# Kernel optimization log

Measured on AMD Instinct MI355X. Metric: run time of the kernel, lower is better.

## Reference

```python
import jax, jax.numpy as jnp
import numpy as np

B, S, H = 4, 2048, 1024
HEADS = 16
DFF = 4 * H
EPS = 1e-12


def _layer_norm(x, w, b):
    mu = jnp.mean(x, axis=-1, keepdims=True)
    var = jnp.mean(jnp.square(x - mu), axis=-1, keepdims=True)
    return (x - mu) * jax.lax.rsqrt(var + EPS) * w + b


def setup_inputs() -> dict:
    key = jax.random.key(0)
    ks = jax.random.split(key, 12)
    sc = 0.02
    return {
        "input": jax.random.normal(ks[0], (B, S, H), dtype=jnp.float32),
        "input_mask": jnp.zeros((B, 1, 1, S), dtype=jnp.float32),
        "norm_w": jnp.ones((H,), jnp.float32),
        "norm_b": jnp.zeros((H,), jnp.float32),
        "qkv_w": sc * jax.random.normal(ks[1], (H, 3 * H), jnp.float32),
        "qkv_b": jnp.zeros((3 * H,), jnp.float32),
        "attn_ow": sc * jax.random.normal(ks[2], (H, H), jnp.float32),
        "attn_ob": jnp.zeros((H,), jnp.float32),
        "attn_nw": jnp.ones((H,), jnp.float32),
        "attn_nb": jnp.zeros((H,), jnp.float32),
        "inter_w": sc * jax.random.normal(ks[3], (H, DFF), jnp.float32),
        "inter_b": jnp.zeros((DFF,), jnp.float32),
        "output_w": sc * jax.random.normal(ks[4], (DFF, H), jnp.float32),
        "output_b": jnp.zeros((H,), jnp.float32),
    }


def reference(input, input_mask, norm_w, norm_b, qkv_w, qkv_b, attn_ow, attn_ob,
              attn_nw, attn_nb, inter_w, inter_b, output_w, output_b):
    b, s, h = input.shape
    hd = h // HEADS
    # pre-LN + fused QKV projection (qkv_func)
    x_ln = _layer_norm(input, norm_w, norm_b)
    qkv = x_ln @ qkv_w + qkv_b                      # [b, s, 3h]
    qkv = qkv.reshape(b, s, 3, HEADS, hd)
    q, k, v = qkv[:, :, 0], qkv[:, :, 1], qkv[:, :, 2]   # [b, s, heads, hd]
    # scaled dot-product attention (flash_attn equivalent, non-causal)
    scale = 1.0 / jnp.sqrt(jnp.float32(hd))
    scores = jnp.einsum('bqnd,bknd->bnqk', q, k) * scale  # [b, heads, s, s]
    scores = scores + input_mask                           # additive mask
    probs = jax.nn.softmax(scores, axis=-1)
    ctx = jnp.einsum('bnqk,bknd->bqnd', probs, v).reshape(b, s, h)
    # attention output projection + residual (mlp_func first half)
    attn_out = ctx @ attn_ow + attn_ob + input
    # post-attention LN + FFN (GELU) + residual
    y = _layer_norm(attn_out, attn_nw, attn_nb)
    y = jax.nn.gelu(y @ inter_w + inter_b, approximate=False)
    return y @ output_w + output_b + attn_out
```

## Files before the change

### kernel.cpp

```cpp
#include <hip/hip_runtime.h>
#include <math.h>

typedef __bf16 bf16_t;
typedef bf16_t bf16x8 __attribute__((ext_vector_type(8)));
typedef bf16_t bf16x4 __attribute__((ext_vector_type(4)));
typedef float f32x4 __attribute__((ext_vector_type(4)));
typedef float f32x16 __attribute__((ext_vector_type(16)));

#define BB 4
#define SS 2048
#define HD1 1024
#define NH 16
#define DFF_ 4096

__device__ __forceinline__ void gload_lds16(const bf16_t* g, bf16_t* l) {
  __builtin_amdgcn_global_load_lds(
      (const __attribute__((address_space(1))) void*)g,
      (__attribute__((address_space(3))) void*)l, 16, 0, 0);
}

__device__ __forceinline__ unsigned pack2_bf16(float a, float b) {
  union { bf16_t h[2]; unsigned u; } cv;
  cv.h[0] = (bf16_t)a;
  cv.h[1] = (bf16_t)b;
  return cv.u;
}

__device__ __forceinline__ float block_reduce_sum(float v, float* red) {
  const int lane = threadIdx.x & 63;
  const int wid = threadIdx.x >> 6;
#pragma unroll
  for (int off = 32; off > 0; off >>= 1) v += __shfl_down(v, off, 64);
  if (lane == 0) red[wid] = v;
  __syncthreads();
  float s = red[0] + red[1] + red[2] + red[3];
  __syncthreads();
  return s;
}

__global__ __launch_bounds__(256) void ln_kernel(const float* __restrict__ x,
                                                 const float* __restrict__ w,
                                                 const float* __restrict__ bv,
                                                 bf16_t* __restrict__ out) {
  __shared__ float red[4];
  const size_t row = blockIdx.x;
  const float4 xv = *(const float4*)(x + row * HD1 + threadIdx.x * 4);
  float s = xv.x + xv.y + xv.z + xv.w;
  s = block_reduce_sum(s, red);
  const float mu = s * (1.0f / HD1);
  float4 d;
  d.x = xv.x - mu; d.y = xv.y - mu; d.z = xv.z - mu; d.w = xv.w - mu;
  float sq = d.x * d.x + d.y * d.y + d.z * d.z + d.w * d.w;
  sq = block_reduce_sum(sq, red);
  const float rs = rsqrtf(sq * (1.0f / HD1) + 1e-12f);
  const float4 wv = *(const float4*)(w + threadIdx.x * 4);
  const float4 bb = *(const float4*)(bv + threadIdx.x * 4);
  bf16x4 o;
  o[0] = (bf16_t)(d.x * rs * wv.x + bb.x);
  o[1] = (bf16_t)(d.y * rs * wv.y + bb.y);
  o[2] = (bf16_t)(d.z * rs * wv.z + bb.z);
  o[3] = (bf16_t)(d.w * rs * wv.w + bb.w);
  *(bf16x4*)(out + row * HD1 + threadIdx.x * 4) = o;
}

__global__ __launch_bounds__(256) void wt_kernel(const float* __restrict__ W,
                                                 bf16_t* __restrict__ Wt,
                                                 int K, int N) {
  __shared__ bf16_t T[32][33];
  const int t = threadIdx.x;
  const int n0 = blockIdx.x * 32, k0 = blockIdx.y * 32;
  const int a = t >> 5, c = t & 31;
#pragma unroll
  for (int i = 0; i < 4; ++i) {
    const int kl = a + i * 8;
    T[kl][c] = (bf16_t)W[(size_t)(k0 + kl) * N + n0 + c];
  }
  __syncthreads();
#pragma unroll
  for (int i = 0; i < 4; ++i) {
    const int nl = a + i * 8;
    Wt[(size_t)(n0 + nl) * K + k0 + c] = T[c][nl];
  }
}

__global__ __launch_bounds__(256) void vtrans_kernel(const bf16_t* __restrict__ qkv,
                                                     bf16_t* __restrict__ Vt) {
  const int t = threadIdx.x;
  const int s = blockIdx.x * 256 + t;
  const int head = blockIdx.y, b = blockIdx.z;
  const bf16_t* src = qkv + (size_t)(b * SS + s) * 3072 + 2048 + head * 64;
  bf16_t* dst = Vt + ((size_t)(b * NH + head) * 64) * SS + s;
#pragma unroll
  for (int j = 0; j < 8; ++j) {
    bf16x8 v = *(const bf16x8*)(src + j * 8);
#pragma unroll
    for (int e = 0; e < 8; ++e) dst[(size_t)(j * 8 + e) * SS] = v[e];
  }
}

#define BAR() __builtin_amdgcn_s_barrier()
#define LGKM0()                                         \
  do {                                                  \
    asm volatile("s_waitcnt lgkmcnt(0)" ::: "memory");  \
    __builtin_amdgcn_sched_barrier(0);                  \
  } while (0)
#define VM4 asm volatile("s_waitcnt vmcnt(4)" ::: "memory")
#define VM0 asm volatile("s_waitcnt vmcnt(0)" ::: "memory")
#define PRIO1 __builtin_amdgcn_s_setprio(1)
#define PRIO0 __builtin_amdgcn_s_setprio(0)

template <int EPI, bool OBF>
__global__ __launch_bounds__(512) void gemm8p(
    const bf16_t* __restrict__ A, const bf16_t* __restrict__ Wt,
    const float* __restrict__ bias, const float* __restrict__ R,
    void* __restrict__ Cout, int M, int N, int K) {
  __shared__ __align__(16) char smem[98304];
  bf16_t* As = (bf16_t*)smem;
  bf16_t* Bs = (bf16_t*)(smem + 32768);

  const int tid = threadIdx.x;
  const int lane = tid & 63;
  const int w = tid >> 6;
  const int l15 = lane & 15, l4 = lane >> 4;
  const int wr = w >> 2;
  const int wc = w & 3;
  const int bh = wc >> 1;
  const int bro = (wc & 1) * 64;

  const int gx = gridDim.x;
  int id = blockIdx.x + gx * blockIdx.y;
  const int cpx = (gx * gridDim.y) >> 3;
  id = (id & 7) * cpx + (id >> 3);
  const int m0 = (id / gx) * 128;
  const int n0 = (id % gx) * 256;

  const int srow = tid >> 3;
  const int scol = (((tid & 7) ^ ((tid >> 3) & 7)) * 8);
  const bf16_t* Ag = A + (size_t)(m0 + srow) * K + scol;
  const bf16_t* Bg = Wt + (size_t)(n0 + srow) * K + scol;
  const size_t K64 = (size_t)64 * K;

  const int chA0 = ((l4) ^ (l15 & 7)) * 8;
  const int chA1 = ((4 + l4) ^ (l15 & 7)) * 8;

#define STA(d, h, t)                                                       \
  gload_lds16(Ag + (size_t)(h)*64 * K + (size_t)(t)*64,                    \
              As + (d)*8192 + (h)*4096 + w * 512)
#define STB(d, h, t)                                                       \
  do {                                                                     \
    gload_lds16(Bg + (size_t)(h)*128 * K + (size_t)(t)*64,                 \
                Bs + (d)*16384 + (h)*8192 + w * 512);                      \
    gload_lds16(Bg + (size_t)(h)*128 * K + K64 + (size_t)(t)*64,           \
                Bs + (d)*16384 + (h)*8192 + 4096 + w * 512);               \
  } while (0)

  bf16x8 af[4][2], bfr[4][2];
  f32x4 acc[4][4] = {};

#define LDA(cur)                                                           \
  do {                                                                     \
    const bf16_t* Ah_ = As + (cur)*8192 + wr * 4096;                       \
    _Pragma("unroll") for (int i_ = 0; i_ < 4; ++i_) {                     \
      af[i_][0] = *(const bf16x8*)(Ah_ + (i_ * 16 + l15) * 64 + chA0);     \
      af[i_][1] = *(const bf16x8*)(Ah_ + (i_ * 16 + l15) * 64 + chA1);     \
    }                                                                      \
  } while (0)
#define LDB(cur, j0)                                                       \
  do {                                                                     \
    const bf16_t* Bh_ = Bs + (cur)*16384 + bh * 8192;                      \
    _Pragma("unroll") for (int j_ = (j0); j_ < (j0) + 2; ++j_) {           \
      bfr[j_][0] = *(const bf16x8*)(Bh_ + (bro + j_ * 16 + l15) * 64 + chA0); \
      bfr[j_][1] = *(const bf16x8*)(Bh_ + (bro + j_ * 16 + l15) * 64 + chA1); \
    }                                                                      \
  } while (0)
#define MM(i0, j0)                                                         \
  do {                                                                     \
    _Pragma("unroll") for (int ks_ = 0; ks_ < 2; ++ks_)                    \
    _Pragma("unroll") for (int i_ = 0; i_ < 2; ++i_)                       \
    _Pragma("unroll") for (int j_ = 0; j_ < 2; ++j_)                       \
        acc[(i0) + i_][(j0) + j_] = __builtin_amdgcn_mfma_f32_16x16x32_bf16( \
            af[(i0) + i_][ks_], bfr[(j0) + j_][ks_],                       \
            acc[(i0) + i_][(j0) + j_], 0, 0, 0);                           \
  } while (0)

  STA(0, 0, 0); STA(0, 1, 0); STB(0, 0, 0); STB(0, 1, 0);
  STA(1, 0, 1); STA(1, 1, 1); STB(1, 0, 1);
  VM4;
  BAR();

  const int NT = K >> 6;
  const int nIter = NT >> 1;
  for (int it = 0; it < nIter; ++it) {
    const int u = 2 * it;
    const bool lastI = (it == nIter - 1);
    LDA(0);
    LDB(0, 0);
    STB(1, 1, u + 1);
    BAR(); LGKM0(); PRIO1; MM(0, 0); PRIO0; BAR();
    LDB(0, 2);
    if (!lastI) STA(0, 0, u + 2);
    BAR(); LGKM0(); PRIO1; MM(2, 0); PRIO0; BAR();
    if (!lastI) STA(0, 1, u + 2);
    BAR(); PRIO1; MM(0, 2); PRIO0; BAR();
    if (!lastI) { STB(0, 0, u + 2); VM4; } else { VM0; }
    BAR(); PRIO1; MM(2, 2); PRIO0; BAR();
    LDA(1);
    LDB(1, 0);
    if (!lastI) STB(0, 1, u + 2);
    BAR(); LGKM0(); PRIO1; MM(0, 0); PRIO0; BAR();
    LDB(1, 2);
    if (!lastI) STA(1, 0, u + 3);
    BAR(); LGKM0(); PRIO1; MM(2, 0); PRIO0; BAR();
    if (!lastI) STA(1, 1, u + 3);
    BAR(); PRIO1; MM(0, 2); PRIO0; BAR();
    if (!lastI) { STB(1, 0, u + 3); VM4; }
    BAR(); PRIO1; MM(2, 2); PRIO0; BAR();
  }
#undef STA
#undef STB
#undef LDA
#undef LDB
#undef MM

  if (OBF) {
    float* Cs = (float*)smem;
    bf16_t* Cb = (bf16_t*)Cout;
    __syncthreads();
#pragma unroll
    for (int p = 0; p < 2; ++p) {
      if (p) __syncthreads();
      if (wr == p) {
#pragma unroll
        for (int i = 0; i < 4; ++i) {
#pragma unroll
          for (int j = 0; j < 4; ++j) {
            const int col = wc * 64 + j * 16 + l15;
            const float bj = bias[n0 + col];
#pragma unroll
            for (int r = 0; r < 4; ++r) {
              float v = acc[i][j][r] + bj;
              if (EPI == 1)
                v = 0.5f * v * (1.0f + erff(v * 0.70710678118654752440f));
              const int lr = i * 16 + l4 * 4 + r;
              const int q = (((col >> 2) ^ (lr & 7)) << 2);
              Cs[lr * 256 + q + (col & 3)] = v;
            }
          }
        }
      }
      __syncthreads();
      const int orow = tid >> 3;
      const int oc = tid & 7;
#pragma unroll
      for (int k = 0; k < 4; ++k) {
        const int col = k * 64 + oc * 8;
        const int q0 = ((((col >> 2) + 0) ^ (orow & 7)) << 2);
        const int q1 = ((((col >> 2) + 1) ^ (orow & 7)) << 2);
        const f32x4 v0 = *(const f32x4*)(Cs + orow * 256 + q0);
        const f32x4 v1 = *(const f32x4*)(Cs + orow * 256 + q1);
        bf16x8 o;
        o[0] = (bf16_t)v0[0]; o[1] = (bf16_t)v0[1];
        o[2] = (bf16_t)v0[2]; o[3] = (bf16_t)v0[3];
        o[4] = (bf16_t)v1[0]; o[5] = (bf16_t)v1[1];
        o[6] = (bf16_t)v1[2]; o[7] = (bf16_t)v1[3];
        *(bf16x8*)(Cb + (size_t)(m0 + p * 64 + orow) * N + n0 + col) = o;
      }
    }
  } else {
    float* Cf = (float*)Cout;
#pragma unroll
    for (int j = 0; j < 4; ++j) {
      const int gn = n0 + wc * 64 + j * 16 + l15;
      const float bj = bias[gn];
#pragma unroll
      for (int i = 0; i < 4; ++i) {
        const int gm = m0 + wr * 64 + i * 16 + l4 * 4;
#pragma unroll
        for (int r = 0; r < 4; ++r) {
          float v = acc[i][j][r] + bj;
          if (EPI == 2) v += R[(size_t)(gm + r) * N + gn];
          Cf[(size_t)(gm + r) * N + gn] = v;
        }
      }
    }
  }
}

__global__ __launch_bounds__(256, 2) void attn_kernel(
    const bf16_t* __restrict__ qkv, const bf16_t* __restrict__ Vt,
    const float* __restrict__ mask, bf16_t* __restrict__ ctx) {
  __shared__ __align__(16) bf16_t K_lds[64 * 72];
  __shared__ __align__(16) bf16_t Vt_lds[64 * 72];
  const int tid = threadIdx.x;
  const int lane = tid & 63;
  const int w = tid >> 6;
  const int l31 = lane & 31;
  const int h = lane >> 5;
  const int q0 = blockIdx.x * 128;
  const int head = blockIdx.y;
  const int b = blockIdx.z;
  const int qrow = q0 + w * 32 + l31;

  bf16x8 qf[4];
  {
    const bf16_t* qp = qkv + (size_t)(b * SS + qrow) * 3072 + head * 64 + 8 * h;
#pragma unroll
    for (int ks = 0; ks < 4; ++ks) qf[ks] = *(const bf16x8*)(qp + 16 * ks);
  }

  const int srow = tid >> 2;
  const int scol = (tid & 3) * 16;

  float m = -3.0e38f, l = 0.0f;
  f32x16 cacc0 = {};
  f32x16 cacc1 = {};

  for (int kv0 = 0; kv0 < SS; kv0 += 64) {
    const bf16_t* kp =
        qkv + (size_t)(b * SS + kv0 + srow) * 3072 + 1024 + head * 64 + scol;
    const bf16_t* vp =
        Vt + ((size_t)(b * NH + head) * 64 + srow) * SS + kv0 + scol;
    const bf16x8 k0 = *(const bf16x8*)kp;
    const bf16x8 k1 = *(const bf16x8*)(kp + 8);
    const bf16x8 v0 = *(const bf16x8*)vp;
    const bf16x8 v1 = *(const bf16x8*)(vp + 8);
    float4 mv[8];
#pragma unroll
    for (int k2 = 0; k2 < 8; ++k2)
      mv[k2] = *(const float4*)(mask + (size_t)b * SS + kv0 + 8 * k2 + 4 * h);
    __syncthreads();
    *(bf16x8*)(K_lds + srow * 72 + scol) = k0;
    *(bf16x8*)(K_lds + srow * 72 + scol + 8) = k1;
    *(bf16x8*)(Vt_lds + srow * 72 + scol) = v0;
    *(bf16x8*)(Vt_lds + srow * 72 + scol + 8) = v1;
    __syncthreads();

    f32x16 sacc0 = {};
    f32x16 sacc1 = {};
#pragma unroll
    for (int ks = 0; ks < 4; ++ks) {
      const bf16x8 kf0 = *(const bf16x8*)(K_lds + l31 * 72 + 16 * ks + 8 * h);
      const bf16x8 kf1 =
          *(const bf16x8*)(K_lds + (l31 + 32) * 72 + 16 * ks + 8 * h);
      sacc0 = __builtin_amdgcn_mfma_f32_32x32x16_bf16(kf0, qf[ks], sacc0, 0, 0, 0);
      sacc1 = __builtin_amdgcn_mfma_f32_32x32x16_bf16(kf1, qf[ks], sacc1, 0, 0, 0);
    }

    float ps[32];
    float tmax = -3.0e38f;
#pragma unroll
    for (int r = 0; r < 16; ++r) {
      const float s0 = sacc0[r] * 0.125f + mv[(r >> 2)][r & 3];
      const float s1 = sacc1[r] * 0.125f + mv[(r >> 2) + 4][r & 3];
      ps[r] = s0;
      ps[16 + r] = s1;
      tmax = fmaxf(tmax, fmaxf(s0, s1));
    }
    tmax = fmaxf(tmax, __shfl_xor(tmax, 32, 64));
    if (__any(tmax > m + 8.0f)) {
      const float mnew = fmaxf(m, tmax);
      const float sc = __expf(m - mnew);
      m = mnew;
      l *= sc;
#pragma unroll
      for (int r = 0; r < 16; ++r) {
        const float scr = __shfl(sc, (r & 3) + 8 * (r >> 2) + 4 * h, 64);
        cacc0[r] *= scr;
        cacc1[r] *= scr;
      }
    }
    float ls = 0.0f;
#pragma unroll
    for (int i = 0; i < 32; ++i) {
      ps[i] = __expf(ps[i] - m);
      ls += ps[i];
    }
    l += ls + __shfl_xor(ls, 32, 64);

    unsigned pw0[8], pw1[8];
#pragma unroll
    for (int k = 0; k < 8; ++k) {
      const int base = (k >> 2) * 16 + (k & 3) * 4;
      pw0[k] = pack2_bf16(ps[base + 0], ps[base + 1]);
      pw1[k] = pack2_bf16(ps[base + 2], ps[base + 3]);
    }
#pragma unroll
    for (int t = 0; t < 4; ++t) {
      const unsigned e0 = h ? pw0[2 * t] : pw0[2 * t + 1];
      const unsigned e1 = h ? pw1[2 * t] : pw1[2 * t + 1];
      const unsigned o0 = (unsigned)__shfl_xor((int)e0, 32, 64);
      const unsigned o1 = (unsigned)__shfl_xor((int)e1, 32, 64);
      const unsigned a0 = h ? pw0[2 * t + 1] : pw0[2 * t];
      const unsigned a1 = h ? pw1[2 * t + 1] : pw1[2 * t];
      union { unsigned u[4]; bf16x8 v; } pu;
      pu.u[0] = h ? o0 : a0;
      pu.u[1] = h ? o1 : a1;
      pu.u[2] = h ? a0 : o0;
      pu.u[3] = h ? a1 : o1;
      const bf16x8 vf0 = *(const bf16x8*)(Vt_lds + l31 * 72 + 16 * t + 8 * h);
      const bf16x8 vf1 =
          *(const bf16x8*)(Vt_lds + (l31 + 32) * 72 + 16 * t + 8 * h);
      cacc0 = __builtin_amdgcn_mfma_f32_32x32x16_bf16(pu.v, vf0, cacc0, 0, 0, 0);
      cacc1 = __builtin_amdgcn_mfma_f32_32x32x16_bf16(pu.v, vf1, cacc1, 0, 0, 0);
    }
  }

  const float linv = 1.0f / l;
#pragma unroll
  for (int r = 0; r < 16; ++r) {
    const int rq = (r & 3) + 8 * (r >> 2) + 4 * h;
    const float li = __shfl(linv, rq, 64);
    const int grow = q0 + w * 32 + rq;
    bf16_t* op = ctx + (size_t)(b * SS + grow) * 1024 + head * 64 + l31;
    op[0] = (bf16_t)(cacc0[r] * li);
    op[32] = (bf16_t)(cacc1[r] * li);
  }
}

extern "C" void kernel_launch(void* const* d_in, const int* in_sizes, int n_in,
                              void* d_out, int out_size, void* d_ws, size_t ws_size,
                              hipStream_t stream) {
  const float* input    = (const float*)d_in[0];
  const float* mask     = (const float*)d_in[1];
  const float* norm_w   = (const float*)d_in[2];
  const float* norm_b   = (const float*)d_in[3];
  const float* qkv_w    = (const float*)d_in[4];
  const float* qkv_b    = (const float*)d_in[5];
  const float* attn_ow  = (const float*)d_in[6];
  const float* attn_ob  = (const float*)d_in[7];
  const float* attn_nw  = (const float*)d_in[8];
  const float* attn_nb  = (const float*)d_in[9];
  const float* inter_w  = (const float*)d_in[10];
  const float* inter_b  = (const float*)d_in[11];
  const float* output_w = (const float*)d_in[12];
  const float* output_b = (const float*)d_in[13];

  char* ws = (char*)d_ws;
  const size_t off_xln = 0;
  const size_t off_qkv = 16777216;
  const size_t off_vt  = 67108864;
  const size_t off_ctx = 83886080;
  const size_t off_ao  = 100663296;
  const size_t off_wq  = 134217728;
  const size_t off_wo  = 140509184;
  const size_t off_wi  = 142606336;
  const size_t off_w2  = 150994944;
  const size_t NEED    = 159383552;
  if (ws_size < NEED) return;

  bf16_t* x_ln  = (bf16_t*)(ws + off_xln);
  bf16_t* qkvb  = (bf16_t*)(ws + off_qkv);
  bf16_t* VtB   = (bf16_t*)(ws + off_vt);
  bf16_t* ctxb  = (bf16_t*)(ws + off_ctx);
  bf16_t* y_ln  = (bf16_t*)(ws + off_ctx);
  float*  a_out = (float*)(ws + off_ao);
  bf16_t* wq_t  = (bf16_t*)(ws + off_wq);
  bf16_t* wo_t  = (bf16_t*)(ws + off_wo);
  bf16_t* wi_t  = (bf16_t*)(ws + off_wi);
  bf16_t* w2_t  = (bf16_t*)(ws + off_w2);
  bf16_t* act   = (bf16_t*)(ws + off_xln);

  const int M = BB * SS;

  wt_kernel<<<dim3(3072 / 32, 1024 / 32), 256, 0, stream>>>(qkv_w, wq_t, 1024, 3072);
  wt_kernel<<<dim3(1024 / 32, 1024 / 32), 256, 0, stream>>>(attn_ow, wo_t, 1024, 1024);
  wt_kernel<<<dim3(4096 / 32, 1024 / 32), 256, 0, stream>>>(inter_w, wi_t, 1024, 4096);
  wt_kernel<<<dim3(1024 / 32, 4096 / 32), 256, 0, stream>>>(output_w, w2_t, 4096, 1024);

  ln_kernel<<<M, 256, 0, stream>>>(input, norm_w, norm_b, x_ln);
  gemm8p<0, true><<<dim3(3072 / 256, M / 128), 512, 0, stream>>>(
      x_ln, wq_t, qkv_b, nullptr, qkvb, M, 3072, 1024);
  vtrans_kernel<<<dim3(SS / 256, NH, BB), 256, 0, stream>>>(qkvb, VtB);
  attn_kernel<<<dim3(SS / 128, NH, BB), 256, 0, stream>>>(qkvb, VtB, mask, ctxb);
  gemm8p<2, false><<<dim3(1024 / 256, M / 128), 512, 0, stream>>>(
      ctxb, wo_t, attn_ob, input, a_out, M, 1024, 1024);
  ln_kernel<<<M, 256, 0, stream>>>(a_out, attn_nw, attn_nb, y_ln);
  gemm8p<1, true><<<dim3(4096 / 256, M / 128), 512, 0, stream>>>(
      y_ln, wi_t, inter_b, nullptr, act, M, 4096, 1024);
  gemm8p<2, false><<<dim3(1024 / 256, M / 128), 512, 0, stream>>>(
      act, w2_t, output_b, a_out, (float*)d_out, M, 1024, 4096);
}
```

Measured before the change: 547.4 us.

## Enlarge GEMM block tile to 256x256 with 8x4 per-warp accumulators

The bf16 GEMM block tile grows from 128x256 to 256x256. Each warp now computes a 128x64 sub-tile with 32 accumulators, and LDS double-buffering is reorganised (128KB shared memory) with a new fragment load and MFMA interleave and adjusted vmcnt waits. The aim is higher arithmetic intensity per LDS and global load and half as many blocks. In exchange register pressure and LDS use rise, which lowers occupancy, and the M=1024 GEMMs get fewer blocks (128), which may underfill the 256 CUs.

```diff
diff --git a/kernel.cpp b/kernel.cpp
--- a/kernel.cpp
+++ b/kernel.cpp
@@ -104,7 +104,8 @@
     asm volatile("s_waitcnt lgkmcnt(0)" ::: "memory");  \
     __builtin_amdgcn_sched_barrier(0);                  \
   } while (0)
-#define VM4 asm volatile("s_waitcnt vmcnt(4)" ::: "memory")
+#define VM8 asm volatile("s_waitcnt vmcnt(8)" ::: "memory")
+#define VM6 asm volatile("s_waitcnt vmcnt(6)" ::: "memory")
 #define VM0 asm volatile("s_waitcnt vmcnt(0)" ::: "memory")
 #define PRIO1 __builtin_amdgcn_s_setprio(1)
 #define PRIO0 __builtin_amdgcn_s_setprio(0)
@@ -114,9 +115,9 @@
     const bf16_t* __restrict__ A, const bf16_t* __restrict__ Wt,
     const float* __restrict__ bias, const float* __restrict__ R,
     void* __restrict__ Cout, int M, int N, int K) {
-  __shared__ __align__(16) char smem[98304];
-  bf16_t* As = (bf16_t*)smem;
-  bf16_t* Bs = (bf16_t*)(smem + 32768);
+  __shared__ __align__(16) char smem[131072];
+  bf16_t* As0 = (bf16_t*)smem;
+  bf16_t* Bs0 = (bf16_t*)(smem + 65536);
 
   const int tid = threadIdx.x;
   const int lane = tid & 63;
@@ -124,68 +125,88 @@
   const int l15 = lane & 15, l4 = lane >> 4;
   const int wr = w >> 2;
   const int wc = w & 3;
-  const int bh = wc >> 1;
-  const int bro = (wc & 1) * 64;
 
   const int gx = gridDim.x;
   int id = blockIdx.x + gx * blockIdx.y;
   const int cpx = (gx * gridDim.y) >> 3;
   id = (id & 7) * cpx + (id >> 3);
-  const int m0 = (id / gx) * 128;
+  const int m0 = (id / gx) * 256;
   const int n0 = (id % gx) * 256;
 
   const int srow = tid >> 3;
   const int scol = (((tid & 7) ^ ((tid >> 3) & 7)) * 8);
   const bf16_t* Ag = A + (size_t)(m0 + srow) * K + scol;
   const bf16_t* Bg = Wt + (size_t)(n0 + srow) * K + scol;
-  const size_t K64 = (size_t)64 * K;
-
-  const int chA0 = ((l4) ^ (l15 & 7)) * 8;
-  const int chA1 = ((4 + l4) ^ (l15 & 7)) * 8;
-
-#define STA(d, h, t)                                                       \
-  gload_lds16(Ag + (size_t)(h)*64 * K + (size_t)(t)*64,                    \
-              As + (d)*8192 + (h)*4096 + w * 512)
-#define STB(d, h, t)                                                       \
-  do {                                                                     \
-    gload_lds16(Bg + (size_t)(h)*128 * K + (size_t)(t)*64,                 \
-                Bs + (d)*16384 + (h)*8192 + w * 512);                      \
-    gload_lds16(Bg + (size_t)(h)*128 * K + K64 + (size_t)(t)*64,           \
-                Bs + (d)*16384 + (h)*8192 + 4096 + w * 512);               \
-  } while (0)
-
-  bf16x8 af[4][2], bfr[4][2];
-  f32x4 acc[4][4] = {};
-
-#define LDA(cur)                                                           \
-  do {                                                                     \
-    const bf16_t* Ah_ = As + (cur)*8192 + wr * 4096;                       \
-    _Pragma("unroll") for (int i_ = 0; i_ < 4; ++i_) {                     \
-      af[i_][0] = *(const bf16x8*)(Ah_ + (i_ * 16 + l15) * 64 + chA0);     \
-      af[i_][1] = *(const bf16x8*)(Ah_ + (i_ * 16 + l15) * 64 + chA1);     \
-    }                                                                      \
-  } while (0)
-#define LDB(cur, j0)                                                       \
-  do {                                                                     \
-    const bf16_t* Bh_ = Bs + (cur)*16384 + bh * 8192;                      \
-    _Pragma("unroll") for (int j_ = (j0); j_ < (j0) + 2; ++j_) {           \
-      bfr[j_][0] = *(const bf16x8*)(Bh_ + (bro + j_ * 16 + l15) * 64 + chA0); \
-      bfr[j_][1] = *(const bf16x8*)(Bh_ + (bro + j_ * 16 + l15) * 64 + chA1); \
-    }                                                                      \
-  } while (0)
-#define MM(i0, j0)                                                         \
-  do {                                                                     \
-    _Pragma("unroll") for (int ks_ = 0; ks_ < 2; ++ks_)                    \
-    _Pragma("unroll") for (int i_ = 0; i_ < 2; ++i_)                       \
-    _Pragma("unroll") for (int j_ = 0; j_ < 2; ++j_)                       \
-        acc[(i0) + i_][(j0) + j_] = __builtin_amdgcn_mfma_f32_16x16x32_bf16( \
-            af[(i0) + i_][ks_], bfr[(j0) + j_][ks_],                       \
-            acc[(i0) + i_][(j0) + j_], 0, 0, 0);                           \
-  } while (0)
-
-  STA(0, 0, 0); STA(0, 1, 0); STB(0, 0, 0); STB(0, 1, 0);
-  STA(1, 0, 1); STA(1, 1, 1); STB(1, 0, 1);
-  VM4;
+
+#define STGA(d, h, t)                                                     \
+  do {                                                                    \
+    gload_lds16(Ag + (size_t)((h)*128) * K + (size_t)(t)*64,              \
+                As0 + (d)*16384 + (h)*8192 + w * 512);                    \
+    gload_lds16(Ag + (size_t)((h)*128 + 64) * K + (size_t)(t)*64,         \
+                As0 + (d)*16384 + (h)*8192 + 4096 + w * 512);             \
+  } while (0)
+#define STGB(d, h, t)                                                     \
+  do {                                                                    \
+    gload_lds16(Bg + (size_t)((h)*128) * K + (size_t)(t)*64,              \
+                Bs0 + (d)*16384 + (h)*8192 + w * 512);                    \
+    gload_lds16(Bg + (size_t)((h)*128 + 64) * K + (size_t)(t)*64,         \
+                Bs0 + (d)*16384 + (h)*8192 + 4096 + w * 512);             \
+  } while (0)
+
+  const int rdA = (wr * 128 + l15) * 64;
+  const int rdB = (wc * 64 + l15) * 64;
+  const int ch0 = ((l4) ^ (l15 & 7)) * 8;
+  const int ch1 = ((4 + l4) ^ (l15 & 7)) * 8;
+
+  bf16x8 afA[4][2], afB[4][2], bfA[2][2], bfB[2][2];
+  f32x4 acc[8][4] = {};
+
+#define LDA03(d)                                                          \
+  do {                                                                    \
+    const bf16_t* p_ = As0 + (d)*16384 + rdA;                             \
+    _Pragma("unroll") for (int i_ = 0; i_ < 4; ++i_) {                    \
+      afA[i_][0] = *(const bf16x8*)(p_ + i_ * 1024 + ch0);                \
+      afA[i_][1] = *(const bf16x8*)(p_ + i_ * 1024 + ch1);                \
+    }                                                                     \
+  } while (0)
+#define LDA47(d)                                                          \
+  do {                                                                    \
+    const bf16_t* p_ = As0 + (d)*16384 + rdA + 4096;                      \
+    _Pragma("unroll") for (int i_ = 0; i_ < 4; ++i_) {                    \
+      afB[i_][0] = *(const bf16x8*)(p_ + i_ * 1024 + ch0);                \
+      afB[i_][1] = *(const bf16x8*)(p_ + i_ * 1024 + ch1);                \
+    }                                                                     \
+  } while (0)
+#define LDB01(d)                                                          \
+  do {                                                                    \
+    const bf16_t* p_ = Bs0 + (d)*16384 + rdB;                             \
+    _Pragma("unroll") for (int j_ = 0; j_ < 2; ++j_) {                    \
+      bfA[j_][0] = *(const bf16x8*)(p_ + j_ * 1024 + ch0);                \
+      bfA[j_][1] = *(const bf16x8*)(p_ + j_ * 1024 + ch1);                \
+    }                                                                     \
+  } while (0)
+#define LDB23(d)                                                          \
+  do {                                                                    \
+    const bf16_t* p_ = Bs0 + (d)*16384 + rdB + 2048;                      \
+    _Pragma("unroll") for (int j_ = 0; j_ < 2; ++j_) {                    \
+      bfB[j_][0] = *(const bf16x8*)(p_ + j_ * 1024 + ch0);                \
+      bfB[j_][1] = *(const bf16x8*)(p_ + j_ * 1024 + ch1);                \
+    }                                                                     \
+  } while (0)
+#define MMQ(AF, BF, IO, JO)                                               \
+  do {                                                                    \
+    _Pragma("unroll") for (int ks_ = 0; ks_ < 2; ++ks_)                   \
+    _Pragma("unroll") for (int i_ = 0; i_ < 4; ++i_)                      \
+    _Pragma("unroll") for (int j_ = 0; j_ < 2; ++j_)                      \
+        acc[(IO) + i_][(JO) + j_] =                                       \
+            __builtin_amdgcn_mfma_f32_16x16x32_bf16(                      \
+                AF[i_][ks_], BF[j_][ks_], acc[(IO) + i_][(JO) + j_],      \
+                0, 0, 0);                                                 \
+  } while (0)
+
+  STGA(0, 0, 0); STGA(0, 1, 0); STGB(0, 0, 0); STGB(0, 1, 0);
+  STGA(1, 0, 1); STGA(1, 1, 1); STGB(1, 0, 1); STGB(1, 1, 1);
+  VM8;
   BAR();
 
   const int NT = K >> 6;
@@ -193,34 +214,34 @@
   for (int it = 0; it < nIter; ++it) {
     const int u = 2 * it;
     const bool lastI = (it == nIter - 1);
-    LDA(0);
-    LDB(0, 0);
-    STB(1, 1, u + 1);
-    BAR(); LGKM0(); PRIO1; MM(0, 0); PRIO0; BAR();
-    LDB(0, 2);
-    if (!lastI) STA(0, 0, u + 2);
-    BAR(); LGKM0(); PRIO1; MM(2, 0); PRIO0; BAR();
-    if (!lastI) STA(0, 1, u + 2);
-    BAR(); PRIO1; MM(0, 2); PRIO0; BAR();
-    if (!lastI) { STB(0, 0, u + 2); VM4; } else { VM0; }
-    BAR(); PRIO1; MM(2, 2); PRIO0; BAR();
-    LDA(1);
-    LDB(1, 0);
-    if (!lastI) STB(0, 1, u + 2);
-    BAR(); LGKM0(); PRIO1; MM(0, 0); PRIO0; BAR();
-    LDB(1, 2);
-    if (!lastI) STA(1, 0, u + 3);
-    BAR(); LGKM0(); PRIO1; MM(2, 0); PRIO0; BAR();
-    if (!lastI) STA(1, 1, u + 3);
-    BAR(); PRIO1; MM(0, 2); PRIO0; BAR();
-    if (!lastI) { STB(1, 0, u + 3); VM4; }
-    BAR(); PRIO1; MM(2, 2); PRIO0; BAR();
-  }
-#undef STA
-#undef STB
-#undef LDA
-#undef LDB
-#undef MM
+    LDA03(0); LDB01(0);
+    if (it > 0) STGB(1, 1, u + 1);
+    BAR(); LGKM0(); PRIO1; MMQ(afA, bfA, 0, 0); PRIO0; BAR();
+    LDA47(0);
+    BAR(); LGKM0(); PRIO1; MMQ(afB, bfA, 4, 0); PRIO0; BAR();
+    LDB23(0);
+    if (!lastI) STGA(0, 0, u + 2);
+    BAR(); LGKM0(); PRIO1; MMQ(afB, bfB, 4, 2); PRIO0; BAR();
+    if (!lastI) { STGA(0, 1, u + 2); STGB(0, 0, u + 2); VM6; } else { VM0; }
+    BAR(); PRIO1; MMQ(afA, bfB, 0, 2); PRIO0; BAR();
+    LDA03(1); LDB01(1);
+    if (!lastI) STGB(0, 1, u + 2);
+    BAR(); LGKM0(); PRIO1; MMQ(afA, bfA, 0, 0); PRIO0; BAR();
+    LDA47(1);
+    BAR(); LGKM0(); PRIO1; MMQ(afB, bfA, 4, 0); PRIO0; BAR();
+    LDB23(1);
+    if (!lastI) STGA(1, 0, u + 3);
+    BAR(); LGKM0(); PRIO1; MMQ(afB, bfB, 4, 2); PRIO0; BAR();
+    if (!lastI) { STGA(1, 1, u + 3); STGB(1, 0, u + 3); VM6; }
+    BAR(); PRIO1; MMQ(afA, bfB, 0, 2); PRIO0; BAR();
+  }
+#undef STGA
+#undef STGB
+#undef LDA03
+#undef LDA47
+#undef LDB01
+#undef LDB23
+#undef MMQ
 
   if (OBF) {
     float* Cs = (float*)smem;
@@ -231,7 +252,7 @@
       if (p) __syncthreads();
       if (wr == p) {
 #pragma unroll
-        for (int i = 0; i < 4; ++i) {
+        for (int i = 0; i < 8; ++i) {
 #pragma unroll
           for (int j = 0; j < 4; ++j) {
             const int col = wc * 64 + j * 16 + l15;
@@ -249,11 +270,11 @@
         }
       }
       __syncthreads();
-      const int orow = tid >> 3;
-      const int oc = tid & 7;
-#pragma unroll
-      for (int k = 0; k < 4; ++k) {
-        const int col = k * 64 + oc * 8;
+      const int orow = tid >> 2;
+      const int oc = (tid & 3) * 64;
+#pragma unroll
+      for (int k = 0; k < 8; ++k) {
+        const int col = oc + k * 8;
         const int q0 = ((((col >> 2) + 0) ^ (orow & 7)) << 2);
         const int q1 = ((((col >> 2) + 1) ^ (orow & 7)) << 2);
         const f32x4 v0 = *(const f32x4*)(Cs + orow * 256 + q0);
@@ -263,7 +284,7 @@
         o[2] = (bf16_t)v0[2]; o[3] = (bf16_t)v0[3];
         o[4] = (bf16_t)v1[0]; o[5] = (bf16_t)v1[1];
         o[6] = (bf16_t)v1[2]; o[7] = (bf16_t)v1[3];
-        *(bf16x8*)(Cb + (size_t)(m0 + p * 64 + orow) * N + n0 + col) = o;
+        *(bf16x8*)(Cb + (size_t)(m0 + p * 128 + orow) * N + n0 + col) = o;
       }
     }
   } else {
@@ -273,8 +294,8 @@
       const int gn = n0 + wc * 64 + j * 16 + l15;
       const float bj = bias[gn];
 #pragma unroll
-      for (int i = 0; i < 4; ++i) {
-        const int gm = m0 + wr * 64 + i * 16 + l4 * 4;
+      for (int i = 0; i < 8; ++i) {
+        const int gm = m0 + wr * 128 + i * 16 + l4 * 4;
 #pragma unroll
         for (int r = 0; r < 4; ++r) {
           float v = acc[i][j][r] + bj;
@@ -468,15 +489,15 @@
   wt_kernel<<<dim3(1024 / 32, 4096 / 32), 256, 0, stream>>>(output_w, w2_t, 4096, 1024);
 
   ln_kernel<<<M, 256, 0, stream>>>(input, norm_w, norm_b, x_ln);
-  gemm8p<0, true><<<dim3(3072 / 256, M / 128), 512, 0, stream>>>(
+  gemm8p<0, true><<<dim3(3072 / 256, M / 256), 512, 0, stream>>>(
       x_ln, wq_t, qkv_b, nullptr, qkvb, M, 3072, 1024);
   vtrans_kernel<<<dim3(SS / 256, NH, BB), 256, 0, stream>>>(qkvb, VtB);
   attn_kernel<<<dim3(SS / 128, NH, BB), 256, 0, stream>>>(qkvb, VtB, mask, ctxb);
-  gemm8p<2, false><<<dim3(1024 / 256, M / 128), 512, 0, stream>>>(
+  gemm8p<2, false><<<dim3(1024 / 256, M / 256), 512, 0, stream>>>(
       ctxb, wo_t, attn_ob, input, a_out, M, 1024, 1024);
   ln_kernel<<<M, 256, 0, stream>>>(a_out, attn_nw, attn_nb, y_ln);
-  gemm8p<1, true><<<dim3(4096 / 256, M / 128), 512, 0, stream>>>(
+  gemm8p<1, true><<<dim3(4096 / 256, M / 256), 512, 0, stream>>>(
       y_ln, wi_t, inter_b, nullptr, act, M, 4096, 1024);
-  gemm8p<2, false><<<dim3(1024 / 256, M / 128), 512, 0, stream>>>(
+  gemm8p<2, false><<<dim3(1024 / 256, M / 256), 512, 0, stream>>>(
       act, w2_t, output_b, a_out, (float*)d_out, M, 1024, 4096);
 }
```

New measurement: 774.1 us. 41.4% more time.
